# Performance work log

Hardware: AMD Instinct MI355X
Metric: run time of the kernel (lower is better)

Reference implementation:

```python
import jax, jax.numpy as jnp
from jax import lax
import numpy as np


def setup_inputs() -> dict:
    key = jax.random.key(0)
    ks = jax.random.split(key, 9)
    B, T, H = 64, 4096, 128
    G = 4 * H
    s = 1.0 / np.sqrt(H)  # PyTorch LSTM default init scale
    return {
        "data": jax.random.normal(ks[0], (B, T, 1), dtype=jnp.float32),
        "h0": jax.random.normal(ks[1], (B, H), dtype=jnp.float32),
        "c0": jax.random.normal(ks[2], (B, H), dtype=jnp.float32),
        "W_ih": jax.random.uniform(ks[3], (G, 1), jnp.float32, -s, s),
        "W_hh": jax.random.uniform(ks[4], (G, H), jnp.float32, -s, s),
        "b_ih": jax.random.uniform(ks[5], (G,), jnp.float32, -s, s),
        "b_hh": jax.random.uniform(ks[6], (G,), jnp.float32, -s, s),
        "W_out": jax.random.uniform(ks[7], (1, H), jnp.float32, -s, s),
        "b_out": jax.random.uniform(ks[8], (1,), jnp.float32, -s, s),
    }


def reference(data, h0, c0, W_ih, W_hh, b_ih, b_hh, W_out, b_out):
    # Single-layer batch-first LSTM (PyTorch gate order i,f,g,o), then Linear on last step.
    H = h0.shape[-1]
    # Precompute input projections for all timesteps: [B, T, 4H] -> time-major [T, B, 4H]
    x_proj = jnp.einsum("bti,gi->btg", data, W_ih) + b_ih + b_hh
    x_proj = jnp.swapaxes(x_proj, 0, 1)

    def step(carry, xg):
        h, c = carry
        gates = xg + h @ W_hh.T  # [B, 4H]
        i = jax.nn.sigmoid(gates[:, 0 * H:1 * H])
        f = jax.nn.sigmoid(gates[:, 1 * H:2 * H])
        g = jnp.tanh(gates[:, 2 * H:3 * H])
        o = jax.nn.sigmoid(gates[:, 3 * H:4 * H])
        c = f * c + i * g
        h = o * jnp.tanh(c)
        return (h, c), None

    (hT, _), _ = lax.scan(step, (h0, c0), x_proj)
    # out[:, -1, :] of the LSTM is hT; final linear projection -> [B, 1]
    return hT @ W_out.T + b_out
```

## Files before the change

kernel.cpp:

```cpp
#include <hip/hip_runtime.h>
#include <math.h>

constexpr int Hdim = 128;
constexpr int TMAX = 4096;

typedef _Float16 v2h __attribute__((ext_vector_type(2)));
typedef _Float16 v8h __attribute__((ext_vector_type(8)));
typedef float v4f __attribute__((ext_vector_type(4)));

#if __has_builtin(__builtin_amdgcn_exp2f)
__device__ __forceinline__ float exp2_fast(float x) {
  return __builtin_amdgcn_exp2f(x);
}
#else
__device__ __forceinline__ float exp2_fast(float x) {
  return __expf(x * 0.6931471805599453f);
}
#endif

__device__ __forceinline__ float rcp_fast(float x) {
  return __builtin_amdgcn_rcpf(x);
}

__device__ __forceinline__ float dot2u(unsigned a, unsigned b, float c) {
#if __has_builtin(__builtin_amdgcn_fdot2)
  return __builtin_amdgcn_fdot2(__builtin_bit_cast(v2h, a),
                                __builtin_bit_cast(v2h, b), c, false);
#else
  const v2h x = __builtin_bit_cast(v2h, a);
  const v2h y = __builtin_bit_cast(v2h, b);
  return fmaf((float)x[0], (float)y[0], fmaf((float)x[1], (float)y[1], c));
#endif
}

__device__ __forceinline__ float sel4(v4f d, int r) {
  const float s01 = (r & 1) ? d.y : d.x;
  const float s23 = (r & 1) ? d.w : d.z;
  return (r & 2) ? s23 : s01;
}

template <int CTRL>
__device__ __forceinline__ float qperm(float v) {
#if __has_builtin(__builtin_amdgcn_update_dpp)
  return __int_as_float(
      __builtin_amdgcn_update_dpp(0, __float_as_int(v), CTRL, 0xF, 0xF, true));
#else
  const int x = (CTRL == 0xB1) ? 1 : (CTRL == 0x4E ? 2 : 3);
  return __shfl_xor(v, x, 64);
#endif
}

typedef unsigned uint;

__global__ __launch_bounds__(512, 2) void lstm_hyb2(
    const float* __restrict__ data, const float* __restrict__ h0,
    const float* __restrict__ c0, const float* __restrict__ W_ih,
    const float* __restrict__ W_hh, const float* __restrict__ b_ih,
    const float* __restrict__ b_hh, const float* __restrict__ W_out,
    const float* __restrict__ b_out, float* __restrict__ out, int T) {
  __shared__ __align__(16) float xs[TMAX];
  __shared__ __align__(16) _Float16 hbuf[2][Hdim];

  const int b = blockIdx.x;
  const int tid = threadIdx.x;
  const int lane = tid & 63;
  const int wv = tid >> 6;
  const bool mrole = (wv < 4);

  {
    const float4* src = (const float4*)(data + (size_t)b * T);
    float4* dst = (float4*)xs;
    for (int i = tid; i < T / 4; i += 512) dst[i] = src[i];
  }

  constexpr float L2E = 1.44269504088896f;

  v8h a[4][4];
  v4f acc_init[4];
  float wihm[4];
  int p = 0, m = 0, r = 0;
  float bias_s = 0.f, wih_s = 0.f;
  int g = 0;

  int el;
  if (mrole) {
    p = lane >> 4;
    m = lane & 15;
    r = m & 3;
    el = 16 * wv + 4 * p + r;
#pragma unroll
    for (int gg = 0; gg < 4; ++gg) {
      const int row = 128 * gg + 16 * wv + m;
      const float Mr = (gg == 2) ? 2.0f * L2E : -L2E;
      const float* wr = W_hh + (size_t)row * Hdim + 8 * p;
#pragma unroll
      for (int c = 0; c < 4; ++c) {
        float4 v0 = ((const float4*)(wr + 32 * c))[0];
        float4 v1 = ((const float4*)(wr + 32 * c))[1];
        a[gg][c] = v8h{(_Float16)(Mr * v0.x), (_Float16)(Mr * v0.y),
                       (_Float16)(Mr * v0.z), (_Float16)(Mr * v0.w),
                       (_Float16)(Mr * v1.x), (_Float16)(Mr * v1.y),
                       (_Float16)(Mr * v1.z), (_Float16)(Mr * v1.w)};
      }
    }
#pragma unroll
    for (int gg = 0; gg < 4; ++gg) {
      const float Mr = (gg == 2) ? 2.0f * L2E : -L2E;
      const int row = 128 * gg + 16 * wv + 4 * p;
      acc_init[gg] = v4f{Mr * (b_ih[row + 0] + b_hh[row + 0]),
                         Mr * (b_ih[row + 1] + b_hh[row + 1]),
                         Mr * (b_ih[row + 2] + b_hh[row + 2]),
                         Mr * (b_ih[row + 3] + b_hh[row + 3])};
      wihm[gg] = Mr * W_ih[128 * gg + el];
    }
  } else {
    const int s = wv - 4;
    g = lane & 3;
    const int local = lane >> 2;
    el = 64 + 16 * s + local;
    const int row = 128 * g + el;
    const float Mr = (g == 2) ? 2.0f * L2E : -L2E;
    const float* wr = W_hh + (size_t)row * Hdim;
#pragma unroll
    for (int j = 0; j < 16; ++j) {
      float4 v0 = ((const float4*)wr)[2 * j];
      float4 v1 = ((const float4*)wr)[2 * j + 1];
      a[j >> 2][j & 3] = v8h{(_Float16)(Mr * v0.x), (_Float16)(Mr * v0.y),
                             (_Float16)(Mr * v0.z), (_Float16)(Mr * v0.w),
                             (_Float16)(Mr * v1.x), (_Float16)(Mr * v1.y),
                             (_Float16)(Mr * v1.z), (_Float16)(Mr * v1.w)};
    }
    bias_s = Mr * (b_ih[row] + b_hh[row]);
    wih_s = Mr * W_ih[row];
  }

  float cst = c0[(size_t)b * Hdim + el];
  if (tid < 128) hbuf[0][tid] = (_Float16)h0[(size_t)b * Hdim + tid];
  __syncthreads();

  for (int t0 = 0; t0 < T; t0 += 4) {
    const float4 xv = *(const float4*)&xs[t0];
    const float xts[4] = {xv.x, xv.y, xv.z, xv.w};
#pragma unroll
    for (int u = 0; u < 4; ++u) {
      const int t = t0 + u;
      const _Float16* hb = hbuf[t & 1];
      _Float16* hn = hbuf[(t + 1) & 1];
      const float xt = xts[u];

      if (mrole) {
        v8h bq[4];
#pragma unroll
        for (int c = 0; c < 4; ++c) bq[c] = *(const v8h*)(hb + 32 * c + 8 * p);

        v4f d0 = __builtin_amdgcn_mfma_f32_16x16x32_f16(a[0][0], bq[0],
                                                        acc_init[0], 0, 0, 0);
        v4f d1 = __builtin_amdgcn_mfma_f32_16x16x32_f16(a[1][0], bq[0],
                                                        acc_init[1], 0, 0, 0);
        v4f d2 = __builtin_amdgcn_mfma_f32_16x16x32_f16(a[2][0], bq[0],
                                                        acc_init[2], 0, 0, 0);
        v4f d3 = __builtin_amdgcn_mfma_f32_16x16x32_f16(a[3][0], bq[0],
                                                        acc_init[3], 0, 0, 0);
#pragma unroll
        for (int c = 1; c < 4; ++c) {
          d0 = __builtin_amdgcn_mfma_f32_16x16x32_f16(a[0][c], bq[c], d0, 0, 0, 0);
          d1 = __builtin_amdgcn_mfma_f32_16x16x32_f16(a[1][c], bq[c], d1, 0, 0, 0);
          d2 = __builtin_amdgcn_mfma_f32_16x16x32_f16(a[2][c], bq[c], d2, 0, 0, 0);
          d3 = __builtin_amdgcn_mfma_f32_16x16x32_f16(a[3][c], bq[c], d3, 0, 0, 0);
        }

        const float zi = sel4(d0, r);
        const float zf = sel4(d1, r);
        const float zg = sel4(d2, r);
        const float zo = sel4(d3, r);

        const float yi = rcp_fast(1.0f + exp2_fast(fmaf(xt, wihm[0], zi)));
        const float yf = rcp_fast(1.0f + exp2_fast(fmaf(xt, wihm[1], zf)));
        const float yg =
            fmaf(-2.0f, rcp_fast(1.0f + exp2_fast(fmaf(xt, wihm[2], zg))), 1.0f);
        const float yo = rcp_fast(1.0f + exp2_fast(fmaf(xt, wihm[3], zo)));

        cst = fmaf(yf, cst, yi * yg);
        const float th = fmaf(
            -2.0f, rcp_fast(1.0f + exp2_fast(cst * (2.0f * L2E))), 1.0f);
        const float h = yo * th;
        if (m < 4) hn[el] = (_Float16)h;
      } else {
        const uint4* hp = (const uint4*)hb;
        uint4 hq[16];
#pragma unroll
        for (int i = 0; i < 16; ++i) hq[i] = hp[i];
#if __has_builtin(__builtin_amdgcn_sched_barrier)
        __builtin_amdgcn_sched_barrier(0);
#endif

        float ac0 = bias_s, ac1 = 0.f, ac2 = 0.f, ac3 = 0.f, ac4 = 0.f,
              ac5 = 0.f, ac6 = 0.f, ac7 = 0.f;
#pragma unroll
        for (int j = 0; j < 16; j += 2) {
          const uint4 wA = __builtin_bit_cast(uint4, a[j >> 2][j & 3]);
          const uint4 wB = __builtin_bit_cast(uint4, a[(j + 1) >> 2][(j + 1) & 3]);
          const uint4 hA = hq[j];
          const uint4 hB = hq[j + 1];
          ac0 = dot2u(wA.x, hA.x, ac0);
          ac1 = dot2u(wA.y, hA.y, ac1);
          ac2 = dot2u(wA.z, hA.z, ac2);
          ac3 = dot2u(wA.w, hA.w, ac3);
          ac4 = dot2u(wB.x, hB.x, ac4);
          ac5 = dot2u(wB.y, hB.y, ac5);
          ac6 = dot2u(wB.z, hB.z, ac6);
          ac7 = dot2u(wB.w, hB.w, ac7);
        }
        const float dsum =
            ((ac0 + ac1) + (ac2 + ac3)) + ((ac4 + ac5) + (ac6 + ac7));

        const float z = fmaf(xt, wih_s, dsum);
        const float uu = rcp_fast(1.0f + exp2_fast(z));

        const float x1 = qperm<0xB1>(uu);
        const float x2 = qperm<0x4E>(uu);
        const float x3 = qperm<0x1B>(uu);

        if (g == 0) {
          const float gg = fmaf(-2.0f, x2, 1.0f);
          cst = fmaf(x1, cst, uu * gg);
          const float th = fmaf(
              -2.0f, rcp_fast(1.0f + exp2_fast(cst * (2.0f * L2E))), 1.0f);
          hn[el] = (_Float16)(x3 * th);
        }
      }
      __syncthreads();
    }
  }

  if (tid < 64) {
    const _Float16* hf = hbuf[T & 1];
    float sum =
        (float)hf[tid] * W_out[tid] + (float)hf[tid + 64] * W_out[tid + 64];
#pragma unroll
    for (int off = 32; off > 0; off >>= 1) sum += __shfl_down(sum, off, 64);
    if (tid == 0) out[b] = sum + b_out[0];
  }
}

extern "C" void kernel_launch(void* const* d_in, const int* in_sizes, int n_in,
                              void* d_out, int out_size, void* d_ws,
                              size_t ws_size, hipStream_t stream) {
  const float* data = (const float*)d_in[0];
  const float* h0 = (const float*)d_in[1];
  const float* c0 = (const float*)d_in[2];
  const float* W_ih = (const float*)d_in[3];
  const float* W_hh = (const float*)d_in[4];
  const float* b_ih = (const float*)d_in[5];
  const float* b_hh = (const float*)d_in[6];
  const float* W_out = (const float*)d_in[7];
  const float* b_out = (const float*)d_in[8];
  float* out = (float*)d_out;

  const int B = in_sizes[1] / Hdim;
  const int T = in_sizes[0] / B;

  lstm_hyb2<<<B, 512, 0, stream>>>(data, h0, c0, W_ih, W_hh, b_ih, b_hh, W_out,
                                   b_out, out, T);
}
```

Baseline: 2.072 ms.

## Split dot-product waves' K dimension across quad lanes with DPP reduction

The dot-product waves now give each lane a quarter of the hidden dimension for all four gates of one element, instead of the full 128-length row of a single gate. Each lane loads only 4 uint4 of h from LDS instead of 16, and the partial sums are combined with quad DPP reductions. Each lane then picks the sum for its own gate before the activation. This cuts per-lane LDS traffic and shortens the serial dot-product chain on the critical path of each timestep. The cost is extra cross-lane reduction steps, with all lanes now doing the cell update redundantly.

```diff
diff --git a/kernel.cpp b/kernel.cpp
--- a/kernel.cpp
+++ b/kernel.cpp
@@ -7,6 +7,7 @@
 typedef _Float16 v2h __attribute__((ext_vector_type(2)));
 typedef _Float16 v8h __attribute__((ext_vector_type(8)));
 typedef float v4f __attribute__((ext_vector_type(4)));
+typedef unsigned uint;
 
 #if __has_builtin(__builtin_amdgcn_exp2f)
 __device__ __forceinline__ float exp2_fast(float x) {
@@ -22,7 +23,7 @@
   return __builtin_amdgcn_rcpf(x);
 }
 
-__device__ __forceinline__ float dot2u(unsigned a, unsigned b, float c) {
+__device__ __forceinline__ float dot2u(uint a, uint b, float c) {
 #if __has_builtin(__builtin_amdgcn_fdot2)
   return __builtin_amdgcn_fdot2(__builtin_bit_cast(v2h, a),
                                 __builtin_bit_cast(v2h, b), c, false);
@@ -50,9 +51,13 @@
 #endif
 }
 
-typedef unsigned uint;
-
-__global__ __launch_bounds__(512, 2) void lstm_hyb2(
+__device__ __forceinline__ float qsum(float v) {
+  v += qperm<0xB1>(v);
+  v += qperm<0x4E>(v);
+  return v;
+}
+
+__global__ __launch_bounds__(512, 2) void lstm_r23(
     const float* __restrict__ data, const float* __restrict__ h0,
     const float* __restrict__ c0, const float* __restrict__ W_ih,
     const float* __restrict__ W_hh, const float* __restrict__ b_ih,
@@ -79,8 +84,9 @@
   v4f acc_init[4];
   float wihm[4];
   int p = 0, m = 0, r = 0;
-  float bias_s = 0.f, wih_s = 0.f;
-  int g = 0;
+  float bias[4] = {0.f, 0.f, 0.f, 0.f};
+  float wihd = 0.f;
+  int cq = 0;
 
   int el;
   if (mrole) {
@@ -89,49 +95,53 @@
     r = m & 3;
     el = 16 * wv + 4 * p + r;
 #pragma unroll
-    for (int gg = 0; gg < 4; ++gg) {
-      const int row = 128 * gg + 16 * wv + m;
-      const float Mr = (gg == 2) ? 2.0f * L2E : -L2E;
+    for (int g = 0; g < 4; ++g) {
+      const int row = 128 * g + 16 * wv + m;
+      const float Mr = (g == 2) ? 2.0f * L2E : -L2E;
       const float* wr = W_hh + (size_t)row * Hdim + 8 * p;
 #pragma unroll
       for (int c = 0; c < 4; ++c) {
         float4 v0 = ((const float4*)(wr + 32 * c))[0];
         float4 v1 = ((const float4*)(wr + 32 * c))[1];
-        a[gg][c] = v8h{(_Float16)(Mr * v0.x), (_Float16)(Mr * v0.y),
-                       (_Float16)(Mr * v0.z), (_Float16)(Mr * v0.w),
-                       (_Float16)(Mr * v1.x), (_Float16)(Mr * v1.y),
-                       (_Float16)(Mr * v1.z), (_Float16)(Mr * v1.w)};
+        a[g][c] = v8h{(_Float16)(Mr * v0.x), (_Float16)(Mr * v0.y),
+                      (_Float16)(Mr * v0.z), (_Float16)(Mr * v0.w),
+                      (_Float16)(Mr * v1.x), (_Float16)(Mr * v1.y),
+                      (_Float16)(Mr * v1.z), (_Float16)(Mr * v1.w)};
       }
     }
 #pragma unroll
-    for (int gg = 0; gg < 4; ++gg) {
-      const float Mr = (gg == 2) ? 2.0f * L2E : -L2E;
-      const int row = 128 * gg + 16 * wv + 4 * p;
-      acc_init[gg] = v4f{Mr * (b_ih[row + 0] + b_hh[row + 0]),
-                         Mr * (b_ih[row + 1] + b_hh[row + 1]),
-                         Mr * (b_ih[row + 2] + b_hh[row + 2]),
-                         Mr * (b_ih[row + 3] + b_hh[row + 3])};
-      wihm[gg] = Mr * W_ih[128 * gg + el];
+    for (int g = 0; g < 4; ++g) {
+      const float Mr = (g == 2) ? 2.0f * L2E : -L2E;
+      const int row = 128 * g + 16 * wv + 4 * p;
+      acc_init[g] = v4f{Mr * (b_ih[row + 0] + b_hh[row + 0]),
+                        Mr * (b_ih[row + 1] + b_hh[row + 1]),
+                        Mr * (b_ih[row + 2] + b_hh[row + 2]),
+                        Mr * (b_ih[row + 3] + b_hh[row + 3])};
+      wihm[g] = Mr * W_ih[128 * g + el];
     }
   } else {
     const int s = wv - 4;
-    g = lane & 3;
-    const int local = lane >> 2;
-    el = 64 + 16 * s + local;
-    const int row = 128 * g + el;
-    const float Mr = (g == 2) ? 2.0f * L2E : -L2E;
-    const float* wr = W_hh + (size_t)row * Hdim;
-#pragma unroll
-    for (int j = 0; j < 16; ++j) {
-      float4 v0 = ((const float4*)wr)[2 * j];
-      float4 v1 = ((const float4*)wr)[2 * j + 1];
-      a[j >> 2][j & 3] = v8h{(_Float16)(Mr * v0.x), (_Float16)(Mr * v0.y),
-                             (_Float16)(Mr * v0.z), (_Float16)(Mr * v0.w),
-                             (_Float16)(Mr * v1.x), (_Float16)(Mr * v1.y),
-                             (_Float16)(Mr * v1.z), (_Float16)(Mr * v1.w)};
-    }
-    bias_s = Mr * (b_ih[row] + b_hh[row]);
-    wih_s = Mr * W_ih[row];
+    const int j = lane >> 2;
+    cq = lane & 3;
+    el = 64 + 16 * s + j;
+#pragma unroll
+    for (int g = 0; g < 4; ++g) {
+      const int row = 128 * g + el;
+      const float Mr = (g == 2) ? 2.0f * L2E : -L2E;
+      const float* wr = W_hh + (size_t)row * Hdim + 32 * cq;
+#pragma unroll
+      for (int c = 0; c < 4; ++c) {
+        float4 v0 = ((const float4*)(wr + 8 * c))[0];
+        float4 v1 = ((const float4*)(wr + 8 * c))[1];
+        a[g][c] = v8h{(_Float16)(Mr * v0.x), (_Float16)(Mr * v0.y),
+                      (_Float16)(Mr * v0.z), (_Float16)(Mr * v0.w),
+                      (_Float16)(Mr * v1.x), (_Float16)(Mr * v1.y),
+                      (_Float16)(Mr * v1.z), (_Float16)(Mr * v1.w)};
+      }
+      bias[g] = (cq == 0) ? Mr * (b_ih[row] + b_hh[row]) : 0.0f;
+    }
+    const float Mq = (cq == 2) ? 2.0f * L2E : -L2E;
+    wihd = Mq * W_ih[128 * cq + el];
   }
 
   float cst = c0[(size_t)b * Hdim + el];
@@ -176,8 +186,8 @@
 
         const float yi = rcp_fast(1.0f + exp2_fast(fmaf(xt, wihm[0], zi)));
         const float yf = rcp_fast(1.0f + exp2_fast(fmaf(xt, wihm[1], zf)));
-        const float yg =
-            fmaf(-2.0f, rcp_fast(1.0f + exp2_fast(fmaf(xt, wihm[2], zg))), 1.0f);
+        const float yg = fmaf(
+            -2.0f, rcp_fast(1.0f + exp2_fast(fmaf(xt, wihm[2], zg))), 1.0f);
         const float yo = rcp_fast(1.0f + exp2_fast(fmaf(xt, wihm[3], zo)));
 
         cst = fmaf(yf, cst, yi * yg);
@@ -187,47 +197,55 @@
         if (m < 4) hn[el] = (_Float16)h;
       } else {
         const uint4* hp = (const uint4*)hb;
-        uint4 hq[16];
-#pragma unroll
-        for (int i = 0; i < 16; ++i) hq[i] = hp[i];
-#if __has_builtin(__builtin_amdgcn_sched_barrier)
-        __builtin_amdgcn_sched_barrier(0);
-#endif
-
-        float ac0 = bias_s, ac1 = 0.f, ac2 = 0.f, ac3 = 0.f, ac4 = 0.f,
-              ac5 = 0.f, ac6 = 0.f, ac7 = 0.f;
-#pragma unroll
-        for (int j = 0; j < 16; j += 2) {
-          const uint4 wA = __builtin_bit_cast(uint4, a[j >> 2][j & 3]);
-          const uint4 wB = __builtin_bit_cast(uint4, a[(j + 1) >> 2][(j + 1) & 3]);
-          const uint4 hA = hq[j];
-          const uint4 hB = hq[j + 1];
-          ac0 = dot2u(wA.x, hA.x, ac0);
-          ac1 = dot2u(wA.y, hA.y, ac1);
-          ac2 = dot2u(wA.z, hA.z, ac2);
-          ac3 = dot2u(wA.w, hA.w, ac3);
-          ac4 = dot2u(wB.x, hB.x, ac4);
-          ac5 = dot2u(wB.y, hB.y, ac5);
-          ac6 = dot2u(wB.z, hB.z, ac6);
-          ac7 = dot2u(wB.w, hB.w, ac7);
+        uint4 hqs[4];
+#pragma unroll
+        for (int i = 0; i < 4; ++i) hqs[i] = hp[4 * cq + i];
+
+        float A0 = bias[0], A1 = bias[1], A2 = bias[2], A3 = bias[3];
+#pragma unroll
+        for (int c = 0; c < 4; ++c) {
+          const uint4 q0 = __builtin_bit_cast(uint4, a[0][c]);
+          const uint4 q1 = __builtin_bit_cast(uint4, a[1][c]);
+          const uint4 q2 = __builtin_bit_cast(uint4, a[2][c]);
+          const uint4 q3 = __builtin_bit_cast(uint4, a[3][c]);
+          const uint4 hh = hqs[c];
+          A0 = dot2u(q0.x, hh.x, A0);
+          A1 = dot2u(q1.x, hh.x, A1);
+          A2 = dot2u(q2.x, hh.x, A2);
+          A3 = dot2u(q3.x, hh.x, A3);
+          A0 = dot2u(q0.y, hh.y, A0);
+          A1 = dot2u(q1.y, hh.y, A1);
+          A2 = dot2u(q2.y, hh.y, A2);
+          A3 = dot2u(q3.y, hh.y, A3);
+          A0 = dot2u(q0.z, hh.z, A0);
+          A1 = dot2u(q1.z, hh.z, A1);
+          A2 = dot2u(q2.z, hh.z, A2);
+          A3 = dot2u(q3.z, hh.z, A3);
+          A0 = dot2u(q0.w, hh.w, A0);
+          A1 = dot2u(q1.w, hh.w, A1);
+          A2 = dot2u(q2.w, hh.w, A2);
+          A3 = dot2u(q3.w, hh.w, A3);
         }
-        const float dsum =
-            ((ac0 + ac1) + (ac2 + ac3)) + ((ac4 + ac5) + (ac6 + ac7));
-
-        const float z = fmaf(xt, wih_s, dsum);
-        const float uu = rcp_fast(1.0f + exp2_fast(z));
+
+        A0 = qsum(A0);
+        A1 = qsum(A1);
+        A2 = qsum(A2);
+        A3 = qsum(A3);
+
+        const float zA = (cq & 1) ? A1 : A0;
+        const float zB = (cq & 1) ? A3 : A2;
+        const float z = (cq & 2) ? zB : zA;
+        const float uu = rcp_fast(1.0f + exp2_fast(fmaf(xt, wihd, z)));
 
         const float x1 = qperm<0xB1>(uu);
         const float x2 = qperm<0x4E>(uu);
         const float x3 = qperm<0x1B>(uu);
 
-        if (g == 0) {
-          const float gg = fmaf(-2.0f, x2, 1.0f);
-          cst = fmaf(x1, cst, uu * gg);
-          const float th = fmaf(
-              -2.0f, rcp_fast(1.0f + exp2_fast(cst * (2.0f * L2E))), 1.0f);
-          hn[el] = (_Float16)(x3 * th);
-        }
+        const float yg = fmaf(-2.0f, x2, 1.0f);
+        cst = fmaf(x1, cst, uu * yg);
+        const float th = fmaf(
+            -2.0f, rcp_fast(1.0f + exp2_fast(cst * (2.0f * L2E))), 1.0f);
+        if (cq == 0) hn[el] = (_Float16)(x3 * th);
       }
       __syncthreads();
     }
@@ -260,6 +278,6 @@
   const int B = in_sizes[1] / Hdim;
   const int T = in_sizes[0] / B;
 
-  lstm_hyb2<<<B, 512, 0, stream>>>(data, h0, c0, W_ih, W_hh, b_ih, b_hh, W_out,
-                                   b_out, out, T);
-}
+  lstm_r23<<<B, 512, 0, stream>>>(data, h0, c0, W_ih, W_hh, b_ih, b_hh, W_out,
+                                  b_out, out, T);
+}
```

New measurement: 2.046 ms. About the same (-1.3%).
